# Performance work log

Hardware: AMD Instinct MI355X
Metric: run time of the kernel (lower is better)

The kernel has to match this reference:

```python
import jax, jax.numpy as jnp
import numpy as np

NODE_F = 8      # node_features
HID = 128       # hidden_dim
HEADS = 8       # nn.MultiheadAttention num_heads
OUT = 256       # output_dim
MAX_ATOMS = 4096  # max_pocket_atoms
NEIGHBOR_RADIUS = 3.0   # _compute_surface_scores neighbor_radius


def setup_inputs() -> dict:
    key = jax.random.key(0)
    ks = jax.random.split(key, 16)
    N, M = 16384, 32
    x = jax.random.normal(ks[0], (N, NODE_F), dtype=jnp.float32)
    pos = jax.random.normal(ks[1], (N, 3), dtype=jnp.float32) * 10.0
    ligand_pos = jax.random.normal(ks[2], (M, 3), dtype=jnp.float32) * 3.0

    def lin(k, fan_in, fan_out):
        return jax.random.normal(k, (fan_in, fan_out), dtype=jnp.float32) / np.sqrt(fan_in)

    return {
        'x': x, 'pos': pos, 'ligand_pos': ligand_pos,
        'W_node': lin(ks[3], NODE_F, HID), 'b_node': jnp.zeros((HID,), jnp.float32),
        'Wq': lin(ks[4], HID, HID), 'bq': jnp.zeros((HID,), jnp.float32),
        'Wk': lin(ks[5], HID, HID), 'bk': jnp.zeros((HID,), jnp.float32),
        'Wv': lin(ks[6], HID, HID), 'bv': jnp.zeros((HID,), jnp.float32),
        'Wo': lin(ks[7], HID, HID), 'bo': jnp.zeros((HID,), jnp.float32),
        'W1': lin(ks[8], HID, OUT), 'b1': jnp.zeros((OUT,), jnp.float32),
        'W2': lin(ks[9], OUT, OUT), 'b2': jnp.zeros((OUT,), jnp.float32),
    }


def _select_binding_site(pos, ligand_pos, k):
    # select_by_binding_site_proximity: distance-to-ligand-center + surface scores, topk
    lig_center = jnp.mean(ligand_pos, axis=0)                       # [3]
    d_lig = jnp.linalg.norm(pos - lig_center, axis=1)               # [N]
    # _compute_surface_scores: cdist(pos,pos) < 3.0, count neighbors (minus self)
    sq = jnp.sum(pos * pos, axis=1)                                 # [N]
    d2 = sq[:, None] + sq[None, :] - 2.0 * (pos @ pos.T)            # [N,N] squared distances
    neighbor_counts = jnp.sum(d2 < NEIGHBOR_RADIUS ** 2, axis=1) - 1
    surface = 1.0 / (neighbor_counts.astype(jnp.float32) + 1.0)
    scores = 1.0 / (1.0 + d_lig / 5.0) + 0.5 * surface
    _, idx = jax.lax.top_k(scores, k)                               # largest=True
    return idx


def reference(x, pos, ligand_pos, W_node, b_node, Wq, bq, Wk, bk, Wv, bv, Wo, bo, W1, b1, W2, b2):
    # N > max_pocket_atoms -> smart selection (adaptive with ligand_pos => binding_site)
    idx = _select_binding_site(pos, ligand_pos, MAX_ATOMS)
    xs = x[idx]                                                     # [K, NODE_F]

    # node embedding (E3 net call fails in the original -> h = node_embedding(x))
    h = xs @ W_node + b_node                                        # [K, HID]

    # MultiheadAttention over the single (batch=None) sequence, eval mode (no dropout)
    K = MAX_ATOMS
    dh = HID // HEADS
    q = (h @ Wq + bq).reshape(K, HEADS, dh).transpose(1, 0, 2)      # [H,K,dh]
    k_ = (h @ Wk + bk).reshape(K, HEADS, dh).transpose(1, 0, 2)
    v = (h @ Wv + bv).reshape(K, HEADS, dh).transpose(1, 0, 2)
    attn = jax.nn.softmax(jnp.einsum('hqd,hkd->hqk', q, k_) / np.sqrt(dh), axis=-1)
    av = jnp.einsum('hqk,hkd->hqd', attn, v).transpose(1, 0, 2).reshape(K, HID)
    h_att = av @ Wo + bo                                            # [K, HID]

    # global mean pool + output projection (Linear-ReLU-Linear)
    pooled = jnp.mean(h_att, axis=0)                                # [HID]
    out = jax.nn.relu(pooled @ W1 + b1) @ W2 + b2                   # [OUT]
    return out
```

## Files before the change

kernel.cpp:

```cpp
#include <hip/hip_runtime.h>
#include <cstdint>
#include <cstddef>

#define NPTS 16384
#define KSEL 4096
#define HIDDEN 128
#define NHEADS 8
#define DHEAD 16
#define OUTD 256
#define NSLICE 4
#define FCAP 262144
#define LCAP 2048
#define TAU 0.15f
#define HROW 264

typedef __attribute__((ext_vector_type(8))) short bf16x8;
typedef __attribute__((ext_vector_type(4))) float f32x4;
typedef __attribute__((ext_vector_type(16))) float f32x16;

#if defined(__has_builtin)
#if __has_builtin(__builtin_amdgcn_exp2f)
#define E2(x) __builtin_amdgcn_exp2f(x)
#endif
#endif
#ifndef E2
#define E2(x) exp2f(x)
#endif

constexpr size_t OFF_PA    = 1024;
constexpr size_t OFF_PB    = OFF_PA  + (size_t)NPTS*32;
constexpr size_t OFF_SQ    = OFF_PB  + (size_t)NPTS*32;
constexpr size_t OFF_DL    = OFF_SQ  + (size_t)NPTS*4;
constexpr size_t OFF_CNT   = OFF_DL  + (size_t)NPTS*4;
constexpr size_t OFF_NFLAG = OFF_CNT + (size_t)NPTS*4;
constexpr size_t OFF_FLG   = OFF_NFLAG + 1024;
constexpr size_t OFF_SEL   = OFF_FLG + (size_t)FCAP*4;
constexpr size_t SZ_PK     = (size_t)NHEADS*KSEL*32*2;
constexpr size_t OFF_QPK   = OFF_SEL + (size_t)KSEL*4;
constexpr size_t OFF_KPK   = OFF_QPK + SZ_PK;
constexpr size_t OFF_V     = OFF_KPK + SZ_PK;
constexpr size_t OFF_LP    = OFF_V  + (size_t)KSEL*HIDDEN*4;
constexpr size_t OFF_WP    = OFF_LP + (size_t)NHEADS*KSEL*NSLICE*4;
constexpr size_t OFF_PAV   = OFF_WP + (size_t)NHEADS*KSEL*NSLICE*4;
constexpr size_t OFF_WSP   = OFF_PAV + 1024;

__device__ __forceinline__ unsigned short f2bf(float f) {
    union { float f; unsigned u; } v; v.f = f;
    unsigned r = v.u + 0x7fffu + ((v.u >> 16) & 1u);
    return (unsigned short)(r >> 16);
}
__device__ __forceinline__ float bf2f(unsigned short h) {
    union { unsigned u; float f; } v; v.u = ((unsigned)h) << 16;
    return v.f;
}

__global__ void __launch_bounds__(256) k_prep(const float* __restrict__ pos, const float* __restrict__ lig, int M,
                       unsigned short* __restrict__ pa, unsigned short* __restrict__ pb,
                       float* __restrict__ sq, float* __restrict__ dl,
                       int* __restrict__ cnt, unsigned int* __restrict__ nflag, float* __restrict__ pav,
                       const float* __restrict__ Wq, const float* __restrict__ Wk, const float* __restrict__ Wv,
                       unsigned short* __restrict__ wsp) {
    __shared__ float ls[128];
    __shared__ float ctr[3];
    int tid = threadIdx.x;
    if (blockIdx.x >= 64) {
        int proj = blockIdx.x - 64;
        const float* W = (proj == 0) ? Wq : ((proj == 1) ? Wk : Wv);
        unsigned short* dst = wsp + (size_t)proj * HIDDEN * 256;
        for (int idx = tid; idx < HIDDEN * HIDDEN; idx += 256) {
            int k = idx >> 7, n = idx & 127;
            float w = W[k * HIDDEN + n];
            unsigned short hi = f2bf(w);
            unsigned short lo = f2bf(w - bf2f(hi));
            dst[(size_t)n * 256 + k] = hi;
            dst[(size_t)n * 256 + 128 + k] = lo;
        }
        return;
    }
    int i = blockIdx.x * 256 + tid;
    cnt[i] = 0;
    if (i == 0) *nflag = 0;
    if (blockIdx.x == 0 && tid < HIDDEN) pav[tid] = 0.f;
    for (int k = tid; k < 3 * M; k += 256) ls[k] = lig[k];
    __syncthreads();
    if (tid < 3) {
        float s = 0.f;
        for (int k = 0; k < M; k++) s += ls[k * 3 + tid];
        ctr[tid] = s / (float)M;
    }
    __syncthreads();
    float x = pos[i*3+0], y = pos[i*3+1], z = pos[i*3+2];
    float s = (x*x + y*y) + z*z;
    sq[i] = s;
    float dx = x - ctr[0], dy = y - ctr[1], dz = z - ctr[2];
    dl[i] = sqrtf((dx*dx + dy*dy) + dz*dz);
    unsigned short xh = f2bf(x); float xr = bf2f(xh); float xl = x - xr;
    unsigned short yh = f2bf(y); float yr = bf2f(yh); float yl = y - yr;
    unsigned short zh = f2bf(z); float zr = bf2f(zh); float zl = z - zr;
    unsigned short xlb = f2bf(xl), ylb = f2bf(yl), zlb = f2bf(zl);
    unsigned short xhA = f2bf(-2.f*xr), xlA = f2bf(-2.f*xl);
    unsigned short yhA = f2bf(-2.f*yr), ylA = f2bf(-2.f*yl);
    unsigned short zhA = f2bf(-2.f*zr), zlA = f2bf(-2.f*zl);
    unsigned short sih = f2bf(s);
    unsigned short sil = f2bf(s - bf2f(sih));
    unsigned short one = f2bf(1.0f);
    union { unsigned short s[16]; float4 f[2]; } A, B;
    A.s[0]=xhA; A.s[1]=xhA; A.s[2]=xlA;
    A.s[3]=yhA; A.s[4]=yhA; A.s[5]=ylA;
    A.s[6]=zhA; A.s[7]=zhA; A.s[8]=zlA;
    A.s[9]=xlA; A.s[10]=ylA; A.s[11]=zlA;
    A.s[12]=sih; A.s[13]=sil; A.s[14]=one; A.s[15]=one;
    B.s[0]=xh;  B.s[1]=xlb;  B.s[2]=xh;
    B.s[3]=yh;  B.s[4]=ylb;  B.s[5]=yh;
    B.s[6]=zh;  B.s[7]=zlb;  B.s[8]=zh;
    B.s[9]=xlb; B.s[10]=ylb; B.s[11]=zlb;
    B.s[12]=one; B.s[13]=one; B.s[14]=sih; B.s[15]=sil;
    float4* pad = (float4*)(pa + (size_t)i * 16);
    pad[0] = A.f[0]; pad[1] = A.f[1];
    float4* pbd = (float4*)(pb + (size_t)i * 16);
    pbd[0] = B.f[0]; pbd[1] = B.f[1];
}

__global__ void __launch_bounds__(256) k_neighbor(
        const unsigned short* __restrict__ pa, const unsigned short* __restrict__ pb,
        int* __restrict__ cnt, unsigned int* __restrict__ flg, unsigned int* __restrict__ nflag) {
    __shared__ unsigned short js[256 * 24];
    __shared__ unsigned int fbuf[LCAP];
    __shared__ unsigned int fcnt, fbase;
    int tid = threadIdx.x;
    if (tid == 0) fcnt = 0;
    int lane = tid & 63, w = tid >> 6;
    int half = lane >> 5, il = lane & 31;
    int i = blockIdx.x * 128 + w * 32 + il;
    bf16x8 bfrag = *(const bf16x8*)(pb + (size_t)i * 16 + half * 8);
    int jb0 = blockIdx.y * 1024;
    int acc = 0;
    for (int chv = 0; chv < 4; chv++) {
        int jb = jb0 + chv * 256;
        __syncthreads();
        {
            const float4* src = (const float4*)(pa + (size_t)(jb + tid) * 16);
            float4 v0 = src[0], v1 = src[1];
            float4* dst = (float4*)&js[tid * 24];
            dst[0] = v0; dst[1] = v1;
        }
        __syncthreads();
        #pragma unroll 2
        for (int t = 0; t < 8; t++) {
            bf16x8 afrag = *(const bf16x8*)&js[(t * 32 + il) * 24 + half * 8];
            f32x16 c = {0.f,0.f,0.f,0.f,0.f,0.f,0.f,0.f,0.f,0.f,0.f,0.f,0.f,0.f,0.f,0.f};
            c = __builtin_amdgcn_mfma_f32_32x32x16_bf16(afrag, bfrag, c, 0, 0, 0);
            int cs = 0, cl = 0;
            #pragma unroll
            for (int r = 0; r < 16; r++) {
                cs += (c[r] < 9.0f - TAU);
                cl += (c[r] < 9.0f + TAU);
            }
            if (cl == cs) {
                acc += cs;
            } else {
                unsigned jt9 = (unsigned)((jb >> 5) + t);
                unsigned xx = atomicAdd(&fcnt, 1u);
                if (xx < LCAP) fbuf[xx] = ((unsigned)i << 10) | (jt9 << 1) | (unsigned)half;
            }
        }
    }
    acc += __shfl_xor(acc, 32);
    if (half == 0) atomicAdd(&cnt[i], acc);
    __syncthreads();
    if (tid == 0) {
        unsigned cf = fcnt; if (cf > LCAP) cf = LCAP;
        fcnt = cf;
        fbase = atomicAdd(nflag, cf);
    }
    __syncthreads();
    unsigned cf = fcnt, fb = fbase;
    for (unsigned xx = tid; xx < cf; xx += 256) {
        unsigned di = fb + xx;
        if (di < FCAP) flg[di] = fbuf[xx];
    }
}

__global__ void __launch_bounds__(256) k_fixup(const float* __restrict__ pos, const float* __restrict__ sq,
        const unsigned int* __restrict__ flg, const unsigned int* __restrict__ nflag,
        int* __restrict__ cnt) {
    int nf = (int)*nflag; if (nf > FCAP) nf = FCAP;
    for (int idx = blockIdx.x * 256 + threadIdx.x; idx < nf; idx += gridDim.x * 256) {
        unsigned pr = flg[idx];
        int i = (int)(pr >> 10);
        int jt = (int)((pr >> 1) & 511u) << 5;
        int half = (int)(pr & 1u);
        float xi = pos[i*3+0], yi = pos[i*3+1], zi = pos[i*3+2];
        float si = sq[i];
        int add = 0;
        #pragma unroll
        for (int r = 0; r < 16; r++) {
            int j = jt + (r & 3) + 8 * (r >> 2) + 4 * half;
            float xj = pos[j*3+0], yj = pos[j*3+1], zj = pos[j*3+2];
            float dot = fmaf(xi, xj, fmaf(yi, yj, zi * zj));
            float d2 = (si + sq[j]) - 2.0f * dot;
            add += (d2 < 9.0f);
        }
        atomicAdd(&cnt[i], add);
    }
}

__global__ void __launch_bounds__(1024) k_select(const float* __restrict__ dl, const int* __restrict__ cnt,
                                                 int* __restrict__ sel) {
    __shared__ unsigned int sk[NPTS];
    __shared__ int hist[256];
    __shared__ int scan2[256];
    __shared__ unsigned int s_prefix;
    __shared__ int s_rem, s_eqtot, s_nout, s_digit, s_cgt;
    int tid = threadIdx.x;
    for (int i = tid; i < NPTS; i += 1024) {
        float score = 1.0f / (1.0f + dl[i] / 5.0f) + 0.5f * (1.0f / (float)cnt[i]);
        unsigned int u = __float_as_uint(score);
        sk[i] = u ^ ((u & 0x80000000u) ? 0xFFFFFFFFu : 0x80000000u);
    }
    if (tid == 0) { s_prefix = 0; s_rem = KSEL; s_nout = 0; s_eqtot = 0; }
    __syncthreads();
    for (int p = 0; p < 4; p++) {
        int sh = 24 - 8 * p;
        if (tid < 256) hist[tid] = 0;
        __syncthreads();
        unsigned int pref = s_prefix;
        int shp = (p == 0) ? 0 : (32 - 8 * p);
        for (int i = tid; i < NPTS; i += 1024) {
            unsigned int key = sk[i];
            bool m = (p == 0) || ((key >> shp) == pref);
            if (m) atomicAdd(&hist[(key >> sh) & 255], 1);
        }
        __syncthreads();
        if (tid < 256) scan2[tid] = hist[tid];
        __syncthreads();
        for (int off = 1; off < 256; off <<= 1) {
            int v = 0;
            if (tid < 256) { v = scan2[tid]; if (tid + off < 256) v += scan2[tid + off]; }
            __syncthreads();
            if (tid < 256) scan2[tid] = v;
            __syncthreads();
        }
        int rem = s_rem;
        if (tid < 256) {
            int hi = scan2[tid];
            int lo = hi - hist[tid];
            if (hi >= rem && lo < rem) { s_digit = tid; s_cgt = lo; }
        }
        __syncthreads();
        if (tid == 0) {
            s_prefix = (s_prefix << 8) | (unsigned int)s_digit;
            s_rem = rem - s_cgt;
            if (p == 3) s_eqtot = hist[s_digit];
        }
        __syncthreads();
    }
    unsigned int T = s_prefix;
    int need_eq = s_rem;
    for (int i = tid; i < NPTS; i += 1024)
        if (sk[i] > T) sel[atomicAdd(&s_nout, 1)] = i;
    __syncthreads();
    if (s_eqtot == need_eq) {
        for (int i = tid; i < NPTS; i += 1024)
            if (sk[i] == T) sel[atomicAdd(&s_nout, 1)] = i;
    } else {
        for (int i = tid; i < NPTS; i += 1024) {
            if (sk[i] == T) {
                int rank = 0;
                for (int j = 0; j < i; j++) rank += (sk[j] == T);
                if (rank < need_eq) sel[atomicAdd(&s_nout, 1)] = i;
            }
        }
    }
}

__global__ void __launch_bounds__(256) k_qkv(const float* __restrict__ x, const int* __restrict__ sel,
        const float* __restrict__ Wn, const float* __restrict__ bn,
        const float* __restrict__ bq, const float* __restrict__ bk, const float* __restrict__ bv,
        const unsigned short* __restrict__ wsp,
        unsigned short* __restrict__ qpk, unsigned short* __restrict__ kpk,
        float* __restrict__ vg) {
    __shared__ float xs[32][8];
    __shared__ unsigned short hsp[32 * HROW];
    int tid = threadIdx.x;
    int r0 = blockIdx.x * 32;
    int proj = blockIdx.y;
    { int rr = tid >> 3, cc = tid & 7; xs[rr][cc] = x[(size_t)sel[r0 + rr] * 8 + cc]; }
    __syncthreads();
    {
        int d = tid & 127, rp = tid >> 7;
        float wn[8];
        #pragma unroll
        for (int c = 0; c < 8; c++) wn[c] = Wn[c * HIDDEN + d];
        float b = bn[d];
        for (int r = rp; r < 32; r += 2) {
            float a = b;
            #pragma unroll
            for (int c = 0; c < 8; c++) a = fmaf(xs[r][c], wn[c], a);
            unsigned short hi = f2bf(a);
            unsigned short lo = f2bf(a - bf2f(hi));
            hsp[r * HROW + d] = hi;
            hsp[r * HROW + 128 + d] = lo;
        }
    }
    __syncthreads();
    int lane = tid & 63, w = tid >> 6;
    int n = lane & 15, g = lane >> 4;
    int rloc = (w & 1) * 16;
    int chalf = w >> 1;
    const unsigned short* wb = wsp + (size_t)proj * HIDDEN * 256;
    const unsigned short* arow = &hsp[(rloc + n) * HROW + ((g < 2) ? 0 : 128) + (g & 1) * 8];
    int b1off = (g & 1) * 8;
    for (int tc = 0; tc < 4; tc++) {
        int col0 = chalf * 64 + tc * 16;
        const unsigned short* bcol = wb + (size_t)(col0 + n) * 256;
        f32x4 acc = {0.f, 0.f, 0.f, 0.f};
        #pragma unroll
        for (int c = 0; c < 8; c++) {
            bf16x8 af = *(const bf16x8*)(arow + c * 16);
            bf16x8 b1 = *(const bf16x8*)(bcol + c * 16 + b1off);
            bf16x8 b2 = {0,0,0,0,0,0,0,0};
            if (g < 2) b2 = *(const bf16x8*)(bcol + 128 + c * 16 + b1off);
            acc = __builtin_amdgcn_mfma_f32_16x16x32_bf16(af, b1, acc, 0, 0, 0);
            acc = __builtin_amdgcn_mfma_f32_16x16x32_bf16(af, b2, acc, 0, 0, 0);
        }
        int col = col0 + n;
        int hh = col >> 4, dd = col & 15;
        if (proj == 0) {
            float bb = bq[col];
            #pragma unroll
            for (int r = 0; r < 4; r++) {
                int qrow = r0 + rloc + g * 4 + r;
                float val = (acc[r] + bb) * 0.36067376022224085f;
                unsigned short hi = f2bf(val);
                unsigned short lo = f2bf(val - bf2f(hi));
                size_t idx = ((size_t)(hh * KSEL) + qrow) * 32 + dd;
                qpk[idx] = hi; qpk[idx + 16] = lo;
            }
        } else if (proj == 1) {
            float bb = bk[col];
            #pragma unroll
            for (int r = 0; r < 4; r++) {
                int qrow = r0 + rloc + g * 4 + r;
                float val = acc[r] + bb;
                unsigned short hi = f2bf(val);
                unsigned short lo = f2bf(val - bf2f(hi));
                size_t idx = ((size_t)(hh * KSEL) + qrow) * 32 + dd;
                kpk[idx] = hi; kpk[idx + 16] = lo;
            }
        } else {
            float bb = bv[col];
            #pragma unroll
            for (int r = 0; r < 4; r++) {
                int qrow = r0 + rloc + g * 4 + r;
                vg[(size_t)qrow * HIDDEN + col] = acc[r] + bb;
            }
        }
    }
}

__global__ void __launch_bounds__(256) k_attn_l(
        const unsigned short* __restrict__ qpk, const unsigned short* __restrict__ kpk,
        float* __restrict__ lp) {
    __shared__ unsigned short smem[256 * 40];
    int tid = threadIdx.x;
    int ks = blockIdx.x, yg = blockIdx.y, h = blockIdx.z;
    size_t hb = (size_t)h * KSEL;
    int lane = tid & 63, w = tid >> 6;
    int n = lane & 31, half = lane >> 5;
    int q0 = yg * 128 + w * 32;
    const unsigned short* qrow = qpk + (hb + q0 + n) * 32;
    bf16x8 aQh = *(const bf16x8*)(qrow + half * 8);
    bf16x8 aQl = *(const bf16x8*)(qrow + 16 + half * 8);
    float lacc[16];
    #pragma unroll
    for (int r = 0; r < 16; r++) lacc[r] = 0.f;
    for (int kc = 0; kc < 4; kc++) {
        __syncthreads();
        {
            int krow = ks * 1024 + kc * 256 + tid;
            const float4* src = (const float4*)(kpk + (hb + krow) * 32);
            float4 a0 = src[0], a1 = src[1], a2 = src[2], a3 = src[3];
            float4* dst = (float4*)&smem[tid * 40];
            dst[0] = a0; dst[1] = a1; dst[2] = a2; dst[3] = a3;
        }
        __syncthreads();
        #pragma unroll 2
        for (int t = 0; t < 8; t++) {
            const unsigned short* rowp = &smem[(t * 32 + n) * 40];
            bf16x8 bKh = *(const bf16x8*)(rowp + half * 8);
            bf16x8 bKl = *(const bf16x8*)(rowp + 16 + half * 8);
            f32x16 c = {0.f,0.f,0.f,0.f,0.f,0.f,0.f,0.f,0.f,0.f,0.f,0.f,0.f,0.f,0.f,0.f};
            c = __builtin_amdgcn_mfma_f32_32x32x16_bf16(aQh, bKh, c, 0, 0, 0);
            c = __builtin_amdgcn_mfma_f32_32x32x16_bf16(aQl, bKh, c, 0, 0, 0);
            c = __builtin_amdgcn_mfma_f32_32x32x16_bf16(aQh, bKl, c, 0, 0, 0);
            #pragma unroll
            for (int r = 0; r < 16; r++) lacc[r] += E2(c[r]);
        }
    }
    #pragma unroll
    for (int m = 1; m < 32; m <<= 1) {
        #pragma unroll
        for (int r = 0; r < 16; r++) lacc[r] += __shfl_xor(lacc[r], m);
    }
    if (n == 0) {
        #pragma unroll
        for (int r = 0; r < 16; r++) {
            int q = q0 + (r & 3) + 8 * (r >> 2) + 4 * half;
            lp[(hb + q) * NSLICE + ks] = lacc[r];
        }
    }
}

__global__ void __launch_bounds__(256) k_attn_w(
        const unsigned short* __restrict__ qpk, const unsigned short* __restrict__ kpk,
        const float* __restrict__ lp, float* __restrict__ wp) {
    __shared__ unsigned short smem[256 * 40];
    __shared__ float rls[256];
    int tid = threadIdx.x;
    int qs = blockIdx.x, yg = blockIdx.y, h = blockIdx.z;
    size_t hb = (size_t)h * KSEL;
    int lane = tid & 63, w = tid >> 6;
    int n = lane & 31, half = lane >> 5;
    int j0 = yg * 128 + w * 32;
    const unsigned short* krow = kpk + (hb + j0 + n) * 32;
    bf16x8 aKh = *(const bf16x8*)(krow + half * 8);
    bf16x8 aKl = *(const bf16x8*)(krow + 16 + half * 8);
    float wacc[16];
    #pragma unroll
    for (int r = 0; r < 16; r++) wacc[r] = 0.f;
    for (int qc = 0; qc < 4; qc++) {
        __syncthreads();
        {
            int qrow = qs * 1024 + qc * 256 + tid;
            const float4* src = (const float4*)(qpk + (hb + qrow) * 32);
            float4 a0 = src[0], a1 = src[1], a2 = src[2], a3 = src[3];
            float4* dst = (float4*)&smem[tid * 40];
            dst[0] = a0; dst[1] = a1; dst[2] = a2; dst[3] = a3;
            float4 p = ((const float4*)lp)[hb + qrow];
            rls[tid] = 1.0f / ((p.x + p.y) + (p.z + p.w));
        }
        __syncthreads();
        #pragma unroll 2
        for (int t = 0; t < 8; t++) {
            const unsigned short* rowp = &smem[(t * 32 + n) * 40];
            bf16x8 bQh = *(const bf16x8*)(rowp + half * 8);
            bf16x8 bQl = *(const bf16x8*)(rowp + 16 + half * 8);
            f32x16 c = {0.f,0.f,0.f,0.f,0.f,0.f,0.f,0.f,0.f,0.f,0.f,0.f,0.f,0.f,0.f,0.f};
            c = __builtin_amdgcn_mfma_f32_32x32x16_bf16(aKh, bQh, c, 0, 0, 0);
            c = __builtin_amdgcn_mfma_f32_32x32x16_bf16(aKl, bQh, c, 0, 0, 0);
            c = __builtin_amdgcn_mfma_f32_32x32x16_bf16(aKh, bQl, c, 0, 0, 0);
            float rv = rls[t * 32 + n];
            #pragma unroll
            for (int r = 0; r < 16; r++) wacc[r] = fmaf(E2(c[r]), rv, wacc[r]);
        }
    }
    #pragma unroll
    for (int m = 1; m < 32; m <<= 1) {
        #pragma unroll
        for (int r = 0; r < 16; r++) wacc[r] += __shfl_xor(wacc[r], m);
    }
    if (n == 0) {
        #pragma unroll
        for (int r = 0; r < 16; r++) {
            int j = j0 + (r & 3) + 8 * (r >> 2) + 4 * half;
            wp[(hb + j) * NSLICE + qs] = wacc[r];
        }
    }
}

__global__ void __launch_bounds__(256) k_colsum(const float* __restrict__ wp, const float* __restrict__ vg,
                                                float* __restrict__ pav) {
    __shared__ float wl[NHEADS][32];
    __shared__ float red[128];
    int tid = threadIdx.x;
    int j0 = blockIdx.x * 32;
    {
        int h = tid >> 5, jl = tid & 31;
        float4 p = ((const float4*)wp)[(size_t)h * KSEL + j0 + jl];
        wl[h][jl] = (p.x + p.y) + (p.z + p.w);
    }
    __syncthreads();
    int d = tid & 127, g = tid >> 7;
    int h = d >> 4;
    float acc = 0.f;
    for (int jl = g * 16; jl < g * 16 + 16; jl++)
        acc = fmaf(wl[h][jl], vg[(size_t)(j0 + jl) * HIDDEN + d], acc);
    if (g == 1) red[d] = acc;
    __syncthreads();
    if (g == 0) atomicAdd(&pav[d], (acc + red[d]) * (1.0f / (float)KSEL));
}

__global__ void __launch_bounds__(256) k_final(const float* __restrict__ pav,
        const float* __restrict__ Wo, const float* __restrict__ bo,
        const float* __restrict__ W1, const float* __restrict__ b1,
        const float* __restrict__ W2, const float* __restrict__ b2,
        float* __restrict__ out) {
    __shared__ float sp[HIDDEN];
    __shared__ float st[OUTD];
    int t = threadIdx.x;
    if (t < HIDDEN) {
        float a = bo[t];
        for (int c = 0; c < HIDDEN; c++) a = fmaf(pav[c], Wo[c * HIDDEN + t], a);
        sp[t] = a;
    }
    __syncthreads();
    {
        float a = b1[t];
        for (int c = 0; c < HIDDEN; c++) a = fmaf(sp[c], W1[c * OUTD + t], a);
        st[t] = fmaxf(a, 0.f);
    }
    __syncthreads();
    {
        float o = b2[t];
        for (int c = 0; c < OUTD; c++) o = fmaf(st[c], W2[c * OUTD + t], o);
        out[t] = o;
    }
}

extern "C" void kernel_launch(void* const* d_in, const int* in_sizes, int n_in,
                              void* d_out, int out_size, void* d_ws, size_t ws_size,
                              hipStream_t stream) {
    (void)n_in; (void)out_size; (void)ws_size;
    const float* x   = (const float*)d_in[0];
    const float* pos = (const float*)d_in[1];
    const float* lig = (const float*)d_in[2];
    const float* Wn  = (const float*)d_in[3];
    const float* bn  = (const float*)d_in[4];
    const float* Wq  = (const float*)d_in[5];
    const float* bq  = (const float*)d_in[6];
    const float* Wk  = (const float*)d_in[7];
    const float* bk  = (const float*)d_in[8];
    const float* Wv  = (const float*)d_in[9];
    const float* bv  = (const float*)d_in[10];
    const float* Wo  = (const float*)d_in[11];
    const float* bo  = (const float*)d_in[12];
    const float* W1  = (const float*)d_in[13];
    const float* b1  = (const float*)d_in[14];
    const float* W2  = (const float*)d_in[15];
    const float* b2  = (const float*)d_in[16];
    int M = in_sizes[2] / 3;

    char* ws = (char*)d_ws;
    unsigned short* pa  = (unsigned short*)(ws + OFF_PA);
    unsigned short* pb  = (unsigned short*)(ws + OFF_PB);
    float*          sq  = (float*)(ws + OFF_SQ);
    float*          dl  = (float*)(ws + OFF_DL);
    int*            cnt = (int*)  (ws + OFF_CNT);
    unsigned int*   nfl = (unsigned int*)(ws + OFF_NFLAG);
    unsigned int*   flg = (unsigned int*)(ws + OFF_FLG);
    int*            sel = (int*)  (ws + OFF_SEL);
    unsigned short* qpk = (unsigned short*)(ws + OFF_QPK);
    unsigned short* kpk = (unsigned short*)(ws + OFF_KPK);
    float*          vg  = (float*)(ws + OFF_V);
    float*          lp  = (float*)(ws + OFF_LP);
    float*          wp  = (float*)(ws + OFF_WP);
    float*          pav = (float*)(ws + OFF_PAV);
    unsigned short* wsp = (unsigned short*)(ws + OFF_WSP);

    hipLaunchKernelGGL(k_prep,     dim3(67),       dim3(256),  0, stream, pos, lig, M, pa, pb, sq, dl, cnt, nfl, pav, Wq, Wk, Wv, wsp);
    hipLaunchKernelGGL(k_neighbor, dim3(128, 16),  dim3(256),  0, stream, pa, pb, cnt, flg, nfl);
    hipLaunchKernelGGL(k_fixup,    dim3(128),      dim3(256),  0, stream, pos, sq, flg, nfl, cnt);
    hipLaunchKernelGGL(k_select,   dim3(1),        dim3(1024), 0, stream, dl, cnt, sel);
    hipLaunchKernelGGL(k_qkv,      dim3(128, 3),   dim3(256),  0, stream, x, sel, Wn, bn, bq, bk, bv, wsp, qpk, kpk, vg);
    hipLaunchKernelGGL(k_attn_l,   dim3(4, 32, 8), dim3(256),  0, stream, qpk, kpk, lp);
    hipLaunchKernelGGL(k_attn_w,   dim3(4, 32, 8), dim3(256),  0, stream, qpk, kpk, lp, wp);
    hipLaunchKernelGGL(k_colsum,   dim3(KSEL/32),  dim3(256),  0, stream, wp, vg, pav);
    hipLaunchKernelGGL(k_final,    dim3(1),        dim3(256),  0, stream, pav, Wo, bo, W1, b1, W2, b2, (float*)d_out);
}
```

Baseline: 276.1 us.

## Drop LDS staging in neighbor/attention kernels and halve k_qkv row tile

The neighbor-count and both attention kernels no longer stage tiles through shared memory with per-chunk barriers. Each wave now loads its MFMA operand fragments straight from global memory, relying on L1/L2 for reuse. In k_attn_w, all 1024 reciprocal row sums are precomputed into LDS once up front. k_qkv now processes 16 rows per block instead of 32 with twice as many blocks, aiming for more parallelism. The trade is fewer barriers and lower LDS use against more global/cache traffic and possible load-latency stalls.

```diff
diff --git a/kernel.cpp b/kernel.cpp
--- a/kernel.cpp
+++ b/kernel.cpp
@@ -124,45 +124,35 @@
 __global__ void __launch_bounds__(256) k_neighbor(
         const unsigned short* __restrict__ pa, const unsigned short* __restrict__ pb,
         int* __restrict__ cnt, unsigned int* __restrict__ flg, unsigned int* __restrict__ nflag) {
-    __shared__ unsigned short js[256 * 24];
     __shared__ unsigned int fbuf[LCAP];
     __shared__ unsigned int fcnt, fbase;
     int tid = threadIdx.x;
     if (tid == 0) fcnt = 0;
+    __syncthreads();
     int lane = tid & 63, w = tid >> 6;
     int half = lane >> 5, il = lane & 31;
     int i = blockIdx.x * 128 + w * 32 + il;
     bf16x8 bfrag = *(const bf16x8*)(pb + (size_t)i * 16 + half * 8);
     int jb0 = blockIdx.y * 1024;
     int acc = 0;
-    for (int chv = 0; chv < 4; chv++) {
-        int jb = jb0 + chv * 256;
-        __syncthreads();
-        {
-            const float4* src = (const float4*)(pa + (size_t)(jb + tid) * 16);
-            float4 v0 = src[0], v1 = src[1];
-            float4* dst = (float4*)&js[tid * 24];
-            dst[0] = v0; dst[1] = v1;
-        }
-        __syncthreads();
-        #pragma unroll 2
-        for (int t = 0; t < 8; t++) {
-            bf16x8 afrag = *(const bf16x8*)&js[(t * 32 + il) * 24 + half * 8];
-            f32x16 c = {0.f,0.f,0.f,0.f,0.f,0.f,0.f,0.f,0.f,0.f,0.f,0.f,0.f,0.f,0.f,0.f};
-            c = __builtin_amdgcn_mfma_f32_32x32x16_bf16(afrag, bfrag, c, 0, 0, 0);
-            int cs = 0, cl = 0;
-            #pragma unroll
-            for (int r = 0; r < 16; r++) {
-                cs += (c[r] < 9.0f - TAU);
-                cl += (c[r] < 9.0f + TAU);
-            }
-            if (cl == cs) {
-                acc += cs;
-            } else {
-                unsigned jt9 = (unsigned)((jb >> 5) + t);
-                unsigned xx = atomicAdd(&fcnt, 1u);
-                if (xx < LCAP) fbuf[xx] = ((unsigned)i << 10) | (jt9 << 1) | (unsigned)half;
-            }
+    #pragma unroll 2
+    for (int t = 0; t < 32; t++) {
+        int row = jb0 + t * 32 + il;
+        bf16x8 afrag = *(const bf16x8*)(pa + (size_t)row * 16 + half * 8);
+        f32x16 c = {0.f,0.f,0.f,0.f,0.f,0.f,0.f,0.f,0.f,0.f,0.f,0.f,0.f,0.f,0.f,0.f};
+        c = __builtin_amdgcn_mfma_f32_32x32x16_bf16(afrag, bfrag, c, 0, 0, 0);
+        int cs = 0, cl = 0;
+        #pragma unroll
+        for (int r = 0; r < 16; r++) {
+            cs += (c[r] < 9.0f - TAU);
+            cl += (c[r] < 9.0f + TAU);
+        }
+        if (cl == cs) {
+            acc += cs;
+        } else {
+            unsigned jt9 = (unsigned)((jb0 >> 5) + t);
+            unsigned xx = atomicAdd(&fcnt, 1u);
+            if (xx < LCAP) fbuf[xx] = ((unsigned)i << 10) | (jt9 << 1) | (unsigned)half;
         }
     }
     acc += __shfl_xor(acc, 32);
@@ -280,12 +270,12 @@
         const unsigned short* __restrict__ wsp,
         unsigned short* __restrict__ qpk, unsigned short* __restrict__ kpk,
         float* __restrict__ vg) {
-    __shared__ float xs[32][8];
-    __shared__ unsigned short hsp[32 * HROW];
-    int tid = threadIdx.x;
-    int r0 = blockIdx.x * 32;
+    __shared__ float xs[16][8];
+    __shared__ unsigned short hsp[16 * HROW];
+    int tid = threadIdx.x;
+    int r0 = blockIdx.x * 16;
     int proj = blockIdx.y;
-    { int rr = tid >> 3, cc = tid & 7; xs[rr][cc] = x[(size_t)sel[r0 + rr] * 8 + cc]; }
+    if (tid < 128) { int rr = tid >> 3, cc = tid & 7; xs[rr][cc] = x[(size_t)sel[r0 + rr] * 8 + cc]; }
     __syncthreads();
     {
         int d = tid & 127, rp = tid >> 7;
@@ -293,7 +283,7 @@
         #pragma unroll
         for (int c = 0; c < 8; c++) wn[c] = Wn[c * HIDDEN + d];
         float b = bn[d];
-        for (int r = rp; r < 32; r += 2) {
+        for (int r = rp; r < 16; r += 2) {
             float a = b;
             #pragma unroll
             for (int c = 0; c < 8; c++) a = fmaf(xs[r][c], wn[c], a);
@@ -306,13 +296,11 @@
     __syncthreads();
     int lane = tid & 63, w = tid >> 6;
     int n = lane & 15, g = lane >> 4;
-    int rloc = (w & 1) * 16;
-    int chalf = w >> 1;
     const unsigned short* wb = wsp + (size_t)proj * HIDDEN * 256;
-    const unsigned short* arow = &hsp[(rloc + n) * HROW + ((g < 2) ? 0 : 128) + (g & 1) * 8];
+    const unsigned short* arow = &hsp[n * HROW + ((g < 2) ? 0 : 128) + (g & 1) * 8];
     int b1off = (g & 1) * 8;
-    for (int tc = 0; tc < 4; tc++) {
-        int col0 = chalf * 64 + tc * 16;
+    for (int tc = 0; tc < 2; tc++) {
+        int col0 = w * 32 + tc * 16;
         const unsigned short* bcol = wb + (size_t)(col0 + n) * 256;
         f32x4 acc = {0.f, 0.f, 0.f, 0.f};
         #pragma unroll
@@ -330,7 +318,7 @@
             float bb = bq[col];
             #pragma unroll
             for (int r = 0; r < 4; r++) {
-                int qrow = r0 + rloc + g * 4 + r;
+                int qrow = r0 + g * 4 + r;
                 float val = (acc[r] + bb) * 0.36067376022224085f;
                 unsigned short hi = f2bf(val);
                 unsigned short lo = f2bf(val - bf2f(hi));
@@ -341,7 +329,7 @@
             float bb = bk[col];
             #pragma unroll
             for (int r = 0; r < 4; r++) {
-                int qrow = r0 + rloc + g * 4 + r;
+                int qrow = r0 + g * 4 + r;
                 float val = acc[r] + bb;
                 unsigned short hi = f2bf(val);
                 unsigned short lo = f2bf(val - bf2f(hi));
@@ -352,7 +340,7 @@
             float bb = bv[col];
             #pragma unroll
             for (int r = 0; r < 4; r++) {
-                int qrow = r0 + rloc + g * 4 + r;
+                int qrow = r0 + g * 4 + r;
                 vg[(size_t)qrow * HIDDEN + col] = acc[r] + bb;
             }
         }
@@ -362,7 +350,6 @@
 __global__ void __launch_bounds__(256) k_attn_l(
         const unsigned short* __restrict__ qpk, const unsigned short* __restrict__ kpk,
         float* __restrict__ lp) {
-    __shared__ unsigned short smem[256 * 40];
     int tid = threadIdx.x;
     int ks = blockIdx.x, yg = blockIdx.y, h = blockIdx.z;
     size_t hb = (size_t)h * KSEL;
@@ -375,28 +362,17 @@
     float lacc[16];
     #pragma unroll
     for (int r = 0; r < 16; r++) lacc[r] = 0.f;
-    for (int kc = 0; kc < 4; kc++) {
-        __syncthreads();
-        {
-            int krow = ks * 1024 + kc * 256 + tid;
-            const float4* src = (const float4*)(kpk + (hb + krow) * 32);
-            float4 a0 = src[0], a1 = src[1], a2 = src[2], a3 = src[3];
-            float4* dst = (float4*)&smem[tid * 40];
-            dst[0] = a0; dst[1] = a1; dst[2] = a2; dst[3] = a3;
-        }
-        __syncthreads();
-        #pragma unroll 2
-        for (int t = 0; t < 8; t++) {
-            const unsigned short* rowp = &smem[(t * 32 + n) * 40];
-            bf16x8 bKh = *(const bf16x8*)(rowp + half * 8);
-            bf16x8 bKl = *(const bf16x8*)(rowp + 16 + half * 8);
-            f32x16 c = {0.f,0.f,0.f,0.f,0.f,0.f,0.f,0.f,0.f,0.f,0.f,0.f,0.f,0.f,0.f,0.f};
-            c = __builtin_amdgcn_mfma_f32_32x32x16_bf16(aQh, bKh, c, 0, 0, 0);
-            c = __builtin_amdgcn_mfma_f32_32x32x16_bf16(aQl, bKh, c, 0, 0, 0);
-            c = __builtin_amdgcn_mfma_f32_32x32x16_bf16(aQh, bKl, c, 0, 0, 0);
-            #pragma unroll
-            for (int r = 0; r < 16; r++) lacc[r] += E2(c[r]);
-        }
+    #pragma unroll 2
+    for (int t = 0; t < 32; t++) {
+        const unsigned short* krow = kpk + (hb + ks * 1024 + t * 32 + n) * 32;
+        bf16x8 bKh = *(const bf16x8*)(krow + half * 8);
+        bf16x8 bKl = *(const bf16x8*)(krow + 16 + half * 8);
+        f32x16 c = {0.f,0.f,0.f,0.f,0.f,0.f,0.f,0.f,0.f,0.f,0.f,0.f,0.f,0.f,0.f,0.f};
+        c = __builtin_amdgcn_mfma_f32_32x32x16_bf16(aQh, bKh, c, 0, 0, 0);
+        c = __builtin_amdgcn_mfma_f32_32x32x16_bf16(aQl, bKh, c, 0, 0, 0);
+        c = __builtin_amdgcn_mfma_f32_32x32x16_bf16(aQh, bKl, c, 0, 0, 0);
+        #pragma unroll
+        for (int r = 0; r < 16; r++) lacc[r] += E2(c[r]);
     }
     #pragma unroll
     for (int m = 1; m < 32; m <<= 1) {
@@ -415,11 +391,14 @@
 __global__ void __launch_bounds__(256) k_attn_w(
         const unsigned short* __restrict__ qpk, const unsigned short* __restrict__ kpk,
         const float* __restrict__ lp, float* __restrict__ wp) {
-    __shared__ unsigned short smem[256 * 40];
-    __shared__ float rls[256];
+    __shared__ float rls[1024];
     int tid = threadIdx.x;
     int qs = blockIdx.x, yg = blockIdx.y, h = blockIdx.z;
     size_t hb = (size_t)h * KSEL;
+    for (int r = tid; r < 1024; r += 256) {
+        float4 p = ((const float4*)lp)[hb + qs * 1024 + r];
+        rls[r] = 1.0f / ((p.x + p.y) + (p.z + p.w));
+    }
     int lane = tid & 63, w = tid >> 6;
     int n = lane & 31, half = lane >> 5;
     int j0 = yg * 128 + w * 32;
@@ -429,31 +408,19 @@
     float wacc[16];
     #pragma unroll
     for (int r = 0; r < 16; r++) wacc[r] = 0.f;
-    for (int qc = 0; qc < 4; qc++) {
-        __syncthreads();
-        {
-            int qrow = qs * 1024 + qc * 256 + tid;
-            const float4* src = (const float4*)(qpk + (hb + qrow) * 32);
-            float4 a0 = src[0], a1 = src[1], a2 = src[2], a3 = src[3];
-            float4* dst = (float4*)&smem[tid * 40];
-            dst[0] = a0; dst[1] = a1; dst[2] = a2; dst[3] = a3;
-            float4 p = ((const float4*)lp)[hb + qrow];
-            rls[tid] = 1.0f / ((p.x + p.y) + (p.z + p.w));
-        }
-        __syncthreads();
-        #pragma unroll 2
-        for (int t = 0; t < 8; t++) {
-            const unsigned short* rowp = &smem[(t * 32 + n) * 40];
-            bf16x8 bQh = *(const bf16x8*)(rowp + half * 8);
-            bf16x8 bQl = *(const bf16x8*)(rowp + 16 + half * 8);
-            f32x16 c = {0.f,0.f,0.f,0.f,0.f,0.f,0.f,0.f,0.f,0.f,0.f,0.f,0.f,0.f,0.f,0.f};
-            c = __builtin_amdgcn_mfma_f32_32x32x16_bf16(aKh, bQh, c, 0, 0, 0);
-            c = __builtin_amdgcn_mfma_f32_32x32x16_bf16(aKl, bQh, c, 0, 0, 0);
-            c = __builtin_amdgcn_mfma_f32_32x32x16_bf16(aKh, bQl, c, 0, 0, 0);
-            float rv = rls[t * 32 + n];
-            #pragma unroll
-            for (int r = 0; r < 16; r++) wacc[r] = fmaf(E2(c[r]), rv, wacc[r]);
-        }
+    __syncthreads();
+    #pragma unroll 2
+    for (int t = 0; t < 32; t++) {
+        const unsigned short* qrow = qpk + (hb + qs * 1024 + t * 32 + n) * 32;
+        bf16x8 bQh = *(const bf16x8*)(qrow + half * 8);
+        bf16x8 bQl = *(const bf16x8*)(qrow + 16 + half * 8);
+        f32x16 c = {0.f,0.f,0.f,0.f,0.f,0.f,0.f,0.f,0.f,0.f,0.f,0.f,0.f,0.f,0.f,0.f};
+        c = __builtin_amdgcn_mfma_f32_32x32x16_bf16(aKh, bQh, c, 0, 0, 0);
+        c = __builtin_amdgcn_mfma_f32_32x32x16_bf16(aKl, bQh, c, 0, 0, 0);
+        c = __builtin_amdgcn_mfma_f32_32x32x16_bf16(aKh, bQl, c, 0, 0, 0);
+        float rv = rls[t * 32 + n];
+        #pragma unroll
+        for (int r = 0; r < 16; r++) wacc[r] = fmaf(E2(c[r]), rv, wacc[r]);
     }
     #pragma unroll
     for (int m = 1; m < 32; m <<= 1) {
@@ -562,7 +529,7 @@
     hipLaunchKernelGGL(k_neighbor, dim3(128, 16),  dim3(256),  0, stream, pa, pb, cnt, flg, nfl);
     hipLaunchKernelGGL(k_fixup,    dim3(128),      dim3(256),  0, stream, pos, sq, flg, nfl, cnt);
     hipLaunchKernelGGL(k_select,   dim3(1),        dim3(1024), 0, stream, dl, cnt, sel);
-    hipLaunchKernelGGL(k_qkv,      dim3(128, 3),   dim3(256),  0, stream, x, sel, Wn, bn, bq, bk, bv, wsp, qpk, kpk, vg);
+    hipLaunchKernelGGL(k_qkv,      dim3(256, 3),   dim3(256),  0, stream, x, sel, Wn, bn, bq, bk, bv, wsp, qpk, kpk, vg);
     hipLaunchKernelGGL(k_attn_l,   dim3(4, 32, 8), dim3(256),  0, stream, qpk, kpk, lp);
     hipLaunchKernelGGL(k_attn_w,   dim3(4, 32, 8), dim3(256),  0, stream, qpk, kpk, lp, wp);
     hipLaunchKernelGGL(k_colsum,   dim3(KSEL/32),  dim3(256),  0, stream, wp, vg, pav);
```

Measured after the change: 280.5 us. Within noise of the previous version (+1.6%).
